# Kernel optimization log

Hardware: AMD Instinct MI355X
Metric: run time of the kernel (lower is better)

## Reference

```python
import jax, jax.numpy as jnp
import numpy as np

N_NODES = 100000
N_EDGES = 1600000
N_GRAPHS = 2000
N_FEAT = 128
HIDDEN = 128
N_LAYERS = 4
BN_EPS = 1e-5


def setup_inputs() -> dict:
    key = jax.random.key(0)
    ks = jax.random.split(key, 8)
    x = jax.random.normal(ks[0], (N_NODES, N_FEAT), dtype=jnp.float32)
    edge_index = jax.random.randint(ks[1], (2, N_EDGES), 0, N_NODES, dtype=jnp.int32)
    batch = jnp.sort(jax.random.randint(ks[2], (N_NODES,), 0, N_GRAPHS, dtype=jnp.int32))
    # layer weights scaled down to keep activations stable over 4 layers
    Ws = jax.random.normal(ks[3], (N_LAYERS, HIDDEN, HIDDEN), dtype=jnp.float32) * 0.1
    bs = jnp.zeros((N_LAYERS, HIDDEN), jnp.float32)
    gammas = jnp.ones((N_LAYERS, HIDDEN), jnp.float32)
    betas = jnp.zeros((N_LAYERS, HIDDEN), jnp.float32)
    run_mean = jnp.zeros((N_LAYERS, HIDDEN), jnp.float32)
    run_var = jnp.ones((N_LAYERS, HIDDEN), jnp.float32)
    W_out = jax.random.normal(ks[4], (HIDDEN, 5), dtype=jnp.float32) * 0.1
    b_out = jnp.zeros((5,), jnp.float32)
    return {"x": x, "edge_index": edge_index, "batch": batch, "Ws": Ws, "bs": bs,
            "gammas": gammas, "betas": betas, "run_mean": run_mean, "run_var": run_var,
            "W_out": W_out, "b_out": b_out}


def _gcn_conv(x, src, dst, norm, self_coef, W, b):
    xw = x @ W                                        # [N, H]
    coef = norm[src] * norm[dst]                      # [E]
    msgs = xw[src] * coef[:, None]                    # [E, H] gather
    agg = jax.ops.segment_sum(msgs, dst, num_segments=N_NODES)  # scatter-add
    agg = agg + xw * self_coef[:, None]               # self-loop term
    return agg + b


def reference(x, edge_index, batch, Ws, bs, gammas, betas, run_mean, run_var, W_out, b_out):
    src, dst = edge_index[0], edge_index[1]
    # degree (incl. self-loop) from destination index
    deg = jax.ops.segment_sum(jnp.ones((N_EDGES,), x.dtype), dst, num_segments=N_NODES) + 1.0
    norm = jax.lax.rsqrt(deg)
    self_coef = norm * norm
    h = x
    for l in range(N_LAYERS):
        h = _gcn_conv(h, src, dst, norm, self_coef, Ws[l], bs[l])
        # BatchNorm1d in eval mode (running stats); dropout is identity in eval
        h = (h - run_mean[l]) * (gammas[l] * jax.lax.rsqrt(run_var[l] + BN_EPS)) + betas[l]
        h = jax.nn.relu(h)
    # global mean pool over graphs
    sums = jax.ops.segment_sum(h, batch, num_segments=N_GRAPHS)
    counts = jax.ops.segment_sum(jnp.ones((N_NODES,), h.dtype), batch, num_segments=N_GRAPHS)
    pooled = sums / jnp.maximum(counts, 1.0)[:, None]  # [G, H]
    return pooled @ W_out + b_out                      # [G, 5]
```

## Files before the change

### kernel.cpp

```cpp
#include <hip/hip_runtime.h>
#include <hip/hip_fp16.h>

#define N_NODES_C 100000
#define N_EDGES_C 1600000
#define N_GRAPHS_C 2000
#define HID 128
#define BN_EPS_C 1e-5f
#define NBUCK 391
#define PART_TILE 4096

typedef _Float16 half8 __attribute__((ext_vector_type(8)));
typedef float float4v __attribute__((ext_vector_type(4)));


__global__ __launch_bounds__(256) void kb_hist(const int* __restrict__ dst, int* __restrict__ bcount) {
    __shared__ int hist[NBUCK];
    const int t = threadIdx.x;
    for (int b = t; b < NBUCK; b += 256) hist[b] = 0;
    __syncthreads();
    const int e0 = blockIdx.x * PART_TILE;
    #pragma unroll
    for (int k = 0; k < 16; k++) {
        int e = e0 + k * 256 + t;
        if (e < N_EDGES_C) atomicAdd(&hist[dst[e] >> 8], 1);
    }
    __syncthreads();
    for (int b = t; b < NBUCK; b += 256) {
        int c = hist[b];
        if (c) atomicAdd(&bcount[b], c);
    }
}

__global__ __launch_bounds__(512) void kb_scan(const int* __restrict__ bcount,
                                               int* __restrict__ bbase, int* __restrict__ bcursor) {
    __shared__ int s[512];
    const int t = threadIdx.x;
    int v = (t < NBUCK) ? bcount[t] : 0;
    s[t] = v;
    __syncthreads();
    for (int off = 1; off < 512; off <<= 1) {
        int u = (t >= off) ? s[t - off] : 0;
        __syncthreads();
        s[t] += u;
        __syncthreads();
    }
    if (t < NBUCK) { int e = s[t] - v; bbase[t] = e; bcursor[t] = e; }
    if (t == 0) bbase[NBUCK] = N_EDGES_C;
}

__global__ __launch_bounds__(256) void kb_part(const int* __restrict__ src, const int* __restrict__ dst,
                                               int* __restrict__ bcursor, int2* __restrict__ ebuf) {
    __shared__ int hist[NBUCK];
    __shared__ int startA[NBUCK];
    __shared__ int lcur[NBUCK];
    const int t = threadIdx.x;
    for (int b = t; b < NBUCK; b += 256) { hist[b] = 0; lcur[b] = 0; }
    __syncthreads();
    const int e0 = blockIdx.x * PART_TILE;
    #pragma unroll
    for (int k = 0; k < 16; k++) {
        int e = e0 + k * 256 + t;
        if (e < N_EDGES_C) atomicAdd(&hist[dst[e] >> 8], 1);
    }
    __syncthreads();
    for (int b = t; b < NBUCK; b += 256) {
        int c = hist[b];
        startA[b] = c ? atomicAdd(&bcursor[b], c) : 0;
    }
    __syncthreads();
    #pragma unroll
    for (int k = 0; k < 16; k++) {
        int e = e0 + k * 256 + t;
        if (e < N_EDGES_C) {
            int d = dst[e];
            int b = d >> 8;
            int pos = startA[b] + atomicAdd(&lcur[b], 1);
            ebuf[pos] = make_int2(src[e], d);
        }
    }
}

__global__ __launch_bounds__(256) void kb_fill(const int2* __restrict__ ebuf, const int* __restrict__ bbase,
                                               int* __restrict__ csr_src, int* __restrict__ offs,
                                               float* __restrict__ norm) {
    __shared__ int s[256];
    __shared__ int excl[256];
    __shared__ int lcur[256];
    const int b = blockIdx.x, t = threadIdx.x;
    const int base = b << 8;
    const int e0 = bbase[b], e1 = bbase[b + 1];
    s[t] = 0; lcur[t] = 0;
    __syncthreads();
    for (int e = e0 + t; e < e1; e += 256)
        atomicAdd(&s[ebuf[e].y & 255], 1);
    __syncthreads();
    int own = s[t];
    for (int off = 1; off < 256; off <<= 1) {
        int v = (t >= off) ? s[t - off] : 0;
        __syncthreads();
        s[t] += v;
        __syncthreads();
    }
    excl[t] = s[t] - own;
    int node = base + t;
    if (node < N_NODES_C) {
        offs[node] = e0 + (s[t] - own);
        norm[node] = rsqrtf((float)own + 1.0f);
    }
    if (b == 0 && t == 0) offs[N_NODES_C] = N_EDGES_C;
    __syncthreads();
    for (int e = e0 + t; e < e1; e += 256) {
        int2 p = ebuf[e];
        int l = p.y & 255;
        int pos = e0 + excl[l] + atomicAdd(&lcur[l], 1);
        csr_src[pos] = p.x;
    }
}


__global__ __launch_bounds__(256) void k_cast(const float* __restrict__ x, _Float16* __restrict__ xh) {
    long i = ((long)blockIdx.x * 256 + threadIdx.x) * 8;
    float4 a = *(const float4*)&x[i];
    float4 b = *(const float4*)&x[i + 4];
    _Float16 p[8] = {(_Float16)a.x, (_Float16)a.y, (_Float16)a.z, (_Float16)a.w,
                     (_Float16)b.x, (_Float16)b.y, (_Float16)b.z, (_Float16)b.w};
    *(half8*)&xh[i] = *(half8*)p;
}

__global__ __launch_bounds__(256) void k_tw(const float* __restrict__ Ws_all, _Float16* __restrict__ WT) {
    int idx = blockIdx.x * 256 + threadIdx.x;
    int l = idx >> 14, r = idx & 16383, k = r >> 7, n = r & 127;
    WT[l * 16384 + n * HID + k] = (_Float16)Ws_all[idx];
}


__global__ __launch_bounds__(256) void k_gemm(const _Float16* __restrict__ Ah,
                                              const _Float16* __restrict__ WT,
                                              const float* __restrict__ norm,
                                              _Float16* __restrict__ Y, int nrows) {
    __shared__ _Float16 Wt[HID][136];
    const int tid = threadIdx.x;
    #pragma unroll
    for (int t = 0; t < 8; t++) {
        int off = tid * 8 + t * 2048;
        half8 v = *(const half8*)&WT[off];
        *(half8*)&Wt[off >> 7][off & 127] = v;
    }
    __syncthreads();

    const int wave = tid >> 6, lane = tid & 63, quad = lane >> 4, l16 = lane & 15;
    half8 Wf[2][4];
    #pragma unroll
    for (int c = 0; c < 2; c++)
        #pragma unroll
        for (int ks = 0; ks < 4; ks++)
            Wf[c][ks] = *(const half8*)&Wt[(wave * 2 + c) * 16 + l16][ks * 32 + quad * 8];

    const int nbase = blockIdx.x * 128;
    #pragma unroll
    for (int t = 0; t < 8; t++) {
        int node = nbase + t * 16 + l16;
        bool ok = node < nrows;
        half8 Af[4];
        const _Float16* arow = Ah + (long)node * HID;
        #pragma unroll
        for (int ks = 0; ks < 4; ks++)
            Af[ks] = ok ? *(const half8*)&arow[ks * 32 + quad * 8] : half8{};
        float4v a0 = {0.f, 0.f, 0.f, 0.f}, a1 = {0.f, 0.f, 0.f, 0.f};
        #pragma unroll
        for (int ks = 0; ks < 4; ks++) {
            a0 = __builtin_amdgcn_mfma_f32_16x16x32_f16(Wf[0][ks], Af[ks], a0, 0, 0, 0);
            a1 = __builtin_amdgcn_mfma_f32_16x16x32_f16(Wf[1][ks], Af[ks], a1, 0, 0, 0);
        }
        if (ok) {
            float nv = norm[node];
            _Float16 p0[4], p1[4];
            #pragma unroll
            for (int r = 0; r < 4; r++) {
                p0[r] = (_Float16)(a0[r] * nv);
                p1[r] = (_Float16)(a1[r] * nv);
            }
            *(ushort4*)&Y[(long)node * HID + (wave * 2 + 0) * 16 + quad * 4] = *(ushort4*)p0;
            *(ushort4*)&Y[(long)node * HID + (wave * 2 + 1) * 16 + quad * 4] = *(ushort4*)p1;
        }
    }
}


__global__ __launch_bounds__(256) void k_agg(const __half* __restrict__ y, const int* __restrict__ offs,
                                             const int* __restrict__ csr_src, const float* __restrict__ norm,
                                             const float* __restrict__ bias, const float* __restrict__ mean,
                                             const float* __restrict__ gamma, const float* __restrict__ var,
                                             const float* __restrict__ beta, __half* __restrict__ h) {
    const int wave = __builtin_amdgcn_readfirstlane(threadIdx.x >> 6);
    const int lane = threadIdx.x & 63;
    const int i = blockIdx.x * 4 + wave;
    const int j = lane * 2;

    float2 f = __half22float2(*(const __half2*)&y[(long)i * HID + j]);
    float acc0 = f.x, acc1 = f.y;

    const int e0 = offs[i], e1 = offs[i + 1];
    int e = e0;
    #define GATHER(EE) { \
        int s_ = csr_src[EE]; \
        float2 g_ = __half22float2(*(const __half2*)&y[(long)s_ * HID + j]); \
        acc0 += g_.x; acc1 += g_.y; }
    for (; e + 8 <= e1; e += 8) {
        GATHER(e) GATHER(e + 1) GATHER(e + 2) GATHER(e + 3)
        GATHER(e + 4) GATHER(e + 5) GATHER(e + 6) GATHER(e + 7)
    }
    for (; e < e1; e++) GATHER(e)
    #undef GATHER

    float ni = norm[i];
    float2 bi = *(const float2*)&bias[j];
    float2 me = *(const float2*)&mean[j];
    float2 ga = *(const float2*)&gamma[j];
    float2 va = *(const float2*)&var[j];
    float2 be = *(const float2*)&beta[j];
    float v0 = (acc0 * ni + bi.x - me.x) * (ga.x * rsqrtf(va.x + BN_EPS_C)) + be.x;
    float v1 = (acc1 * ni + bi.y - me.y) * (ga.y * rsqrtf(va.y + BN_EPS_C)) + be.y;
    *(__half2*)&h[(long)i * HID + j] = __floats2half2_rn(fmaxf(v0, 0.f), fmaxf(v1, 0.f));
}


__global__ __launch_bounds__(128) void k_pool(const __half* __restrict__ h, const int* __restrict__ batch,
                                              float* __restrict__ psum, int* __restrict__ pcount) {
    const int j = threadIdx.x;
    const int i0 = blockIdx.x * 128;
    const int iend = min(i0 + 128, N_NODES_C);
    if (i0 >= N_NODES_C) return;
    float acc = 0.f;
    int cur = batch[i0];
    int runStart = i0;
    for (int i = i0; i < iend; i++) {
        int g = batch[i];
        if (g != cur) {
            atomicAdd(&psum[(long)cur * HID + j], acc);
            if (j == 0) atomicAdd(&pcount[cur], i - runStart);
            acc = 0.f; cur = g; runStart = i;
        }
        acc += __half2float(h[(long)i * HID + j]);
    }
    atomicAdd(&psum[(long)cur * HID + j], acc);
    if (j == 0) atomicAdd(&pcount[cur], iend - runStart);
}

__global__ __launch_bounds__(128) void k_final(const float* __restrict__ psum, const int* __restrict__ pcount,
                                               const float* __restrict__ W_out, const float* __restrict__ b_out,
                                               float* __restrict__ out) {
    __shared__ float red[128][5];
    const int g = blockIdx.x, j = threadIdx.x;
    float cnt = fmaxf((float)pcount[g], 1.f);
    float p = psum[(long)g * HID + j] / cnt;
    #pragma unroll
    for (int o = 0; o < 5; o++) red[j][o] = p * W_out[j * 5 + o];
    __syncthreads();
    for (int off = 64; off >= 1; off >>= 1) {
        if (j < off) {
            #pragma unroll
            for (int o = 0; o < 5; o++) red[j][o] += red[j + off][o];
        }
        __syncthreads();
    }
    if (j < 5) out[g * 5 + j] = red[0][j] + b_out[j];
}


extern "C" void kernel_launch(void* const* d_in, const int* in_sizes, int n_in,
                              void* d_out, int out_size, void* d_ws, size_t ws_size,
                              hipStream_t stream) {
    const float* x        = (const float*)d_in[0];
    const int*   eidx     = (const int*)d_in[1];
    const int*   src      = eidx;
    const int*   dst      = eidx + N_EDGES_C;
    const int*   batch    = (const int*)d_in[2];
    const float* Ws_all   = (const float*)d_in[3];
    const float* bs       = (const float*)d_in[4];
    const float* gammas   = (const float*)d_in[5];
    const float* betas    = (const float*)d_in[6];
    const float* run_mean = (const float*)d_in[7];
    const float* run_var  = (const float*)d_in[8];
    const float* W_out    = (const float*)d_in[9];
    const float* b_out    = (const float*)d_in[10];
    float* out = (float*)d_out;

    char* wp = (char*)d_ws;
    auto alloc = [&](size_t bytes) { char* p = wp; wp += (bytes + 255) & ~(size_t)255; return p; };
    __half*   h       = (__half*)alloc((size_t)N_NODES_C * HID * 2);
    _Float16* y       = (_Float16*)alloc((size_t)N_NODES_C * HID * 2);
    int2*     ebuf    = (int2*)y;
    _Float16* xh      = (_Float16*)alloc((size_t)N_NODES_C * HID * 2);
    _Float16* WT      = (_Float16*)alloc((size_t)4 * HID * HID * 2);
    int*      csr_src = (int*)alloc((size_t)N_EDGES_C * 4);
    int*      offs    = (int*)alloc((size_t)(N_NODES_C + 1) * 4);
    float*    norm    = (float*)alloc((size_t)N_NODES_C * 4);
    int*      bcount  = (int*)alloc((NBUCK + 1) * 4);
    int*      bbase   = (int*)alloc((NBUCK + 1) * 4);
    int*      bcursor = (int*)alloc((NBUCK + 1) * 4);
    float*    psum    = (float*)alloc((size_t)N_GRAPHS_C * HID * 4);
    int*      pcount  = (int*)alloc((size_t)N_GRAPHS_C * 4);

    hipMemsetAsync(bcount, 0, (NBUCK + 1) * 4, stream);
    hipMemsetAsync(psum,   0, (size_t)N_GRAPHS_C * HID * 4, stream);
    hipMemsetAsync(pcount, 0, (size_t)N_GRAPHS_C * 4, stream);

    k_cast<<<(N_NODES_C * HID) / 2048, 256, 0, stream>>>(x, xh);
    k_tw  <<<256, 256, 0, stream>>>(Ws_all, WT);

    const int PB = (N_EDGES_C + PART_TILE - 1) / PART_TILE;
    kb_hist<<<PB, 256, 0, stream>>>(dst, bcount);
    kb_scan<<<1, 512, 0, stream>>>(bcount, bbase, bcursor);
    kb_part<<<PB, 256, 0, stream>>>(src, dst, bcursor, ebuf);
    kb_fill<<<NBUCK, 256, 0, stream>>>(ebuf, bbase, csr_src, offs, norm);

    const int GB = (N_NODES_C + 127) / 128;
    const int AB = (N_NODES_C + 3) / 4;
    for (int l = 0; l < 4; l++) {
        const _Float16* A = (l == 0) ? xh : (const _Float16*)h;
        k_gemm<<<GB, 256, 0, stream>>>(A, WT + (size_t)l * HID * HID, norm, y, N_NODES_C);
        k_agg<<<AB, 256, 0, stream>>>((const __half*)y, offs, csr_src, norm,
                                      bs + l * HID, run_mean + l * HID, gammas + l * HID,
                                      run_var + l * HID, betas + l * HID, h);
    }
    k_pool <<<GB, 128, 0, stream>>>(h, batch, psum, pcount);
    k_final<<<N_GRAPHS_C, 128, 0, stream>>>(psum, pcount, W_out, b_out, out);
}
```

Measured before the change: 558.2 us.

## Gather 16-byte half8 rows with four edge groups per wave in aggregation

The aggregation kernel now splits each wave into four 16-lane groups. Each lane loads 8 halves (16 bytes) per neighbor, so the wave processes four edges at once instead of one edge with 4-byte loads. Partial sums are reduced across the groups with cross-lane shuffles, and one group applies the bias, batchnorm and ReLU epilogue. The aim is wider loads and more memory-level parallelism in the gather; the costs are a masked tail, shuffle reductions and three of the four groups sitting idle during the epilogue.

```diff
diff --git a/kernel.cpp b/kernel.cpp
--- a/kernel.cpp
+++ b/kernel.cpp
@@ -187,41 +187,78 @@
 }
 
 
-__global__ __launch_bounds__(256) void k_agg(const __half* __restrict__ y, const int* __restrict__ offs,
+__global__ __launch_bounds__(256) void k_agg(const _Float16* __restrict__ y, const int* __restrict__ offs,
                                              const int* __restrict__ csr_src, const float* __restrict__ norm,
                                              const float* __restrict__ bias, const float* __restrict__ mean,
                                              const float* __restrict__ gamma, const float* __restrict__ var,
-                                             const float* __restrict__ beta, __half* __restrict__ h) {
-    const int wave = __builtin_amdgcn_readfirstlane(threadIdx.x >> 6);
+                                             const float* __restrict__ beta, _Float16* __restrict__ h) {
+    const int wave = threadIdx.x >> 6;
     const int lane = threadIdx.x & 63;
-    const int i = blockIdx.x * 4 + wave;
-    const int j = lane * 2;
-
-    float2 f = __half22float2(*(const __half2*)&y[(long)i * HID + j]);
-    float acc0 = f.x, acc1 = f.y;
+    const int g  = lane >> 4;
+    const int sl = lane & 15;
+    const int c  = sl << 3;
+    const int i  = blockIdx.x * 4 + wave;
 
     const int e0 = offs[i], e1 = offs[i + 1];
+    const _Float16* __restrict__ yc = y + c;
+
+    float acc[8] = {0.f, 0.f, 0.f, 0.f, 0.f, 0.f, 0.f, 0.f};
+
+    if (g == 0) {
+        half8 v = *(const half8*)&yc[(long)i * HID];
+        #pragma unroll
+        for (int r = 0; r < 8; r++) acc[r] += (float)v[r];
+    }
+
     int e = e0;
-    #define GATHER(EE) { \
-        int s_ = csr_src[EE]; \
-        float2 g_ = __half22float2(*(const __half2*)&y[(long)s_ * HID + j]); \
-        acc0 += g_.x; acc1 += g_.y; }
-    for (; e + 8 <= e1; e += 8) {
-        GATHER(e) GATHER(e + 1) GATHER(e + 2) GATHER(e + 3)
-        GATHER(e + 4) GATHER(e + 5) GATHER(e + 6) GATHER(e + 7)
-    }
-    for (; e < e1; e++) GATHER(e)
-    #undef GATHER
-
-    float ni = norm[i];
-    float2 bi = *(const float2*)&bias[j];
-    float2 me = *(const float2*)&mean[j];
-    float2 ga = *(const float2*)&gamma[j];
-    float2 va = *(const float2*)&var[j];
-    float2 be = *(const float2*)&beta[j];
-    float v0 = (acc0 * ni + bi.x - me.x) * (ga.x * rsqrtf(va.x + BN_EPS_C)) + be.x;
-    float v1 = (acc1 * ni + bi.y - me.y) * (ga.y * rsqrtf(va.y + BN_EPS_C)) + be.y;
-    *(__half2*)&h[(long)i * HID + j] = __floats2half2_rn(fmaxf(v0, 0.f), fmaxf(v1, 0.f));
+    while (e + 16 <= e1) {
+        int s0 = csr_src[e + g];
+        int s1 = csr_src[e + g + 4];
+        int s2 = csr_src[e + g + 8];
+        int s3 = csr_src[e + g + 12];
+        half8 v0 = *(const half8*)&yc[(long)s0 * HID];
+        half8 v1 = *(const half8*)&yc[(long)s1 * HID];
+        half8 v2 = *(const half8*)&yc[(long)s2 * HID];
+        half8 v3 = *(const half8*)&yc[(long)s3 * HID];
+        #pragma unroll
+        for (int r = 0; r < 8; r++)
+            acc[r] += ((float)v0[r] + (float)v1[r]) + ((float)v2[r] + (float)v3[r]);
+        e += 16;
+    }
+    if (e < e1) {
+        const int q = e1 - 1;
+        int r0 = e + g, r1 = r0 + 4, r2 = r0 + 8, r3 = r0 + 12;
+        int s0 = csr_src[min(r0, q)];
+        int s1 = csr_src[min(r1, q)];
+        int s2 = csr_src[min(r2, q)];
+        int s3 = csr_src[min(r3, q)];
+        half8 v0 = half8{}, v1 = half8{}, v2 = half8{}, v3 = half8{};
+        if (r0 < e1) v0 = *(const half8*)&yc[(long)s0 * HID];
+        if (r1 < e1) v1 = *(const half8*)&yc[(long)s1 * HID];
+        if (r2 < e1) v2 = *(const half8*)&yc[(long)s2 * HID];
+        if (r3 < e1) v3 = *(const half8*)&yc[(long)s3 * HID];
+        #pragma unroll
+        for (int r = 0; r < 8; r++)
+            acc[r] += ((float)v0[r] + (float)v1[r]) + ((float)v2[r] + (float)v3[r]);
+    }
+
+    #pragma unroll
+    for (int r = 0; r < 8; r++) {
+        acc[r] += __shfl_xor(acc[r], 16);
+        acc[r] += __shfl_xor(acc[r], 32);
+    }
+
+    if (g == 0) {
+        const float ni = norm[i];
+        _Float16 p[8];
+        #pragma unroll
+        for (int r = 0; r < 8; r++) {
+            int j = c + r;
+            float v = (acc[r] * ni + bias[j] - mean[j]) * (gamma[j] * rsqrtf(var[j] + BN_EPS_C)) + beta[j];
+            p[r] = (_Float16)fmaxf(v, 0.f);
+        }
+        *(half8*)&h[(long)i * HID + c] = *(half8*)p;
+    }
 }
 
 
@@ -320,10 +357,10 @@
     for (int l = 0; l < 4; l++) {
         const _Float16* A = (l == 0) ? xh : (const _Float16*)h;
         k_gemm<<<GB, 256, 0, stream>>>(A, WT + (size_t)l * HID * HID, norm, y, N_NODES_C);
-        k_agg<<<AB, 256, 0, stream>>>((const __half*)y, offs, csr_src, norm,
+        k_agg<<<AB, 256, 0, stream>>>((const _Float16*)y, offs, csr_src, norm,
                                       bs + l * HID, run_mean + l * HID, gammas + l * HID,
-                                      run_var + l * HID, betas + l * HID, h);
-    }
-    k_pool <<<GB, 128, 0, stream>>>(h, batch, psum, pcount);
+                                      run_var + l * HID, betas + l * HID, (_Float16*)h);
+    }
+    k_pool <<<GB, 128, 0, stream>>>((const __half*)h, batch, psum, pcount);
     k_final<<<N_GRAPHS_C, 128, 0, stream>>>(psum, pcount, W_out, b_out, out);
 }
```

Measured after the change: 573.5 us. 2.7% more time.
